# Kernel tuning notes

Hardware: AMD Instinct MI355X
Metric: run time of the kernel (lower is better)

Reference implementation:

```python
import jax, jax.numpy as jnp
import numpy as np

EPS = 1e-8


def householder_matrix(vs, dim):
    """Sequentially apply Householder reflections: Q <- (I - 2 v v^T / ||v||^2) Q."""
    def body(Q, v):
        coef = 2.0 / (jnp.sum(v * v) + EPS)
        Q = Q - coef * jnp.outer(v, v @ Q)
        return Q, None
    Q0 = jnp.eye(dim, dtype=vs.dtype)
    Q, _ = jax.lax.scan(body, Q0, vs)
    return Q


def _rotate_half(x):
    x1, x2 = jnp.split(x, 2, axis=-1)
    return jnp.concatenate((-x2, x1), axis=-1)


def setup_inputs() -> dict:
    key = jax.random.key(0)
    kq, kk, kc, ks, kv = jax.random.split(key, 5)
    B, H, S, D = 4, 16, 4096, 64
    q = jax.random.normal(kq, (B, H, S, D), dtype=jnp.float32)
    k = jax.random.normal(kk, (B, H, S, D), dtype=jnp.float32)
    cos = jax.random.uniform(kc, (B, S, D), dtype=jnp.float32)
    sin = jax.random.uniform(ks, (B, S, D), dtype=jnp.float32)
    vs = jax.random.normal(kv, (D // 2, D), dtype=jnp.float32) * 0.02
    return {"q": q, "k": k, "cos": cos, "sin": sin, "vs": vs}


def reference(q, k, cos, sin, vs):
    D = q.shape[-1]
    Q = householder_matrix(vs, D)            # [D, D], orthogonal
    # inverse rotation: x @ Q^T
    qi = q @ Q.T
    ki = k @ Q.T
    cos_b = cos[:, None, :, :]               # [B,1,S,D]
    sin_b = sin[:, None, :, :]
    q_rot = qi * cos_b + _rotate_half(qi) * sin_b
    k_rot = ki * cos_b + _rotate_half(ki) * sin_b
    # forward rotation: x @ Q
    return q_rot @ Q, k_rot @ Q
```

## Files before the change

### kernel.cpp

```cpp
#include <hip/hip_runtime.h>

typedef __attribute__((ext_vector_type(8))) short short8;
typedef __attribute__((ext_vector_type(4))) float floatx4;
typedef unsigned short u16;
typedef unsigned int   u32;

__device__ __forceinline__ u32 f2bf(float f) {
  u32 u = __float_as_uint(f);
  return (u + 0x7fffu + ((u >> 16) & 1u)) >> 16;
}

__device__ __forceinline__ short8 cvt8v(float4 a, float4 b) {
  short8 r;
  r[0] = (short)f2bf(a.x); r[1] = (short)f2bf(a.y); r[2] = (short)f2bf(a.z); r[3] = (short)f2bf(a.w);
  r[4] = (short)f2bf(b.x); r[5] = (short)f2bf(b.y); r[6] = (short)f2bf(b.z); r[7] = (short)f2bf(b.w);
  return r;
}

#define QB_OFF  0
#define QT_OFF  9216
#define COS_OFF 18432
#define SIN_OFF 22784
#define SH_OFF  27136
#define SV_OFF  18432

__global__ void __launch_bounds__(256, 4) rnrope_fused(
    const float* __restrict__ qp, const float* __restrict__ kp,
    const float* __restrict__ cosp, const float* __restrict__ sinp,
    const float* __restrict__ vsp, float* __restrict__ outp) {
  __shared__ __align__(16) char smem[36352];
  u16*   qb = (u16*)(smem + QB_OFF);
  u16*   qt = (u16*)(smem + QT_OFF);
  float* cs = (float*)(smem + COS_OFF);
  float* sn = (float*)(smem + SIN_OFF);
  float* sv = (float*)(smem + SV_OFF);

  const int tid  = threadIdx.x;
  const int lane = tid & 63;
  const int t    = lane & 15;
  const int quad = lane >> 4;
  const int wave = tid >> 6;
  u16* shw = (u16*)(smem + SH_OFF) + wave * 1152;

  const int b  = blockIdx.x >> 8;
  const int st = blockIdx.x & 255;
  const int s  = st << 4;

  *(float4*)(sv + tid * 8)     = *(const float4*)(vsp + tid * 8);
  *(float4*)(sv + tid * 8 + 4) = *(const float4*)(vsp + tid * 8 + 4);
  const int tk  = tid >> 4;
  const int off = (tid & 15) << 2;
  const float4 creg = *(const float4*)(cosp + (((b << 12) + s + tk) << 6) + off);
  const float4 sreg = *(const float4*)(sinp + (((b << 12) + s + tk) << 6) + off);
  __syncthreads();

  if (wave == 0) {
    const int j = lane;
    float col[64];
#pragma unroll
    for (int i = 0; i < 64; i++) col[i] = (i == j) ? 1.f : 0.f;
#pragma unroll 1
    for (int r = 0; r < 32; r++) {
      const float* vr = sv + r * 64;
      float vv0 = 0, vv1 = 0, vv2 = 0, vv3 = 0, w0 = 0, w1 = 0, w2 = 0, w3 = 0;
#pragma unroll
      for (int i = 0; i < 64; i += 4) {
        float4 v4 = *(const float4*)(vr + i);
        vv0 += v4.x * v4.x; vv1 += v4.y * v4.y; vv2 += v4.z * v4.z; vv3 += v4.w * v4.w;
        w0 += v4.x * col[i]; w1 += v4.y * col[i + 1]; w2 += v4.z * col[i + 2]; w3 += v4.w * col[i + 3];
      }
      float coef = 2.f / (((vv0 + vv1) + (vv2 + vv3)) + 1e-8f);
      float cw = coef * ((w0 + w1) + (w2 + w3));
#pragma unroll
      for (int i = 0; i < 64; i += 4) {
        float4 v4 = *(const float4*)(vr + i);
        col[i]     -= v4.x * cw;
        col[i + 1] -= v4.y * cw;
        col[i + 2] -= v4.z * cw;
        col[i + 3] -= v4.w * cw;
      }
    }
#pragma unroll
    for (int i = 0; i < 64; i += 2) {
      u16 v0 = (u16)f2bf(col[i]);
      u16 v1 = (u16)f2bf(col[i + 1]);
      qb[(i) * 72 + j]     = v0;
      qb[(i + 1) * 72 + j] = v1;
      *(u32*)&qt[j * 72 + i] = (u32)v0 | ((u32)v1 << 16);
    }
  }
  __syncthreads();
  *(float4*)(cs + tk * 68 + off) = creg;
  *(float4*)(sn + tk * 68 + off) = sreg;
  __syncthreads();

  const int hbase = b << 4;
  auto xptr = [&](int c) -> const float* {
    const float* base = (c < 16) ? qp : kp;
    return base + ((((hbase + (c & 15)) << 12) + s + t) << 6);
  };

  const int c0 = wave << 3;
  float4 n0, n1, n2, n3;
  {
    const float* p = xptr(c0);
    n0 = *(const float4*)(p + quad * 8);
    n1 = *(const float4*)(p + quad * 8 + 4);
    n2 = *(const float4*)(p + 32 + quad * 8);
    n3 = *(const float4*)(p + 32 + quad * 8 + 4);
  }

#pragma unroll 1
  for (int it = 0; it < 8; ++it) {
    const int c = c0 + it;
    float4 x0 = n0, x1 = n1, x2 = n2, x3 = n3;
    if (it < 7) {
      const float* p = xptr(c + 1);
      n0 = *(const float4*)(p + quad * 8);
      n1 = *(const float4*)(p + quad * 8 + 4);
      n2 = *(const float4*)(p + 32 + quad * 8);
      n3 = *(const float4*)(p + 32 + quad * 8 + 4);
    }
    short8 bq0 = cvt8v(x0, x1);
    short8 bq1 = cvt8v(x2, x3);

    int qoff = 0;
    asm volatile("" : "+v"(qoff));

    floatx4 acc[4];
#pragma unroll
    for (int i0 = 0; i0 < 4; i0++) {
      short8 a0 = *(const short8*)(qb + qoff + (i0 * 16 + t) * 72 + quad * 8);
      short8 a1 = *(const short8*)(qb + qoff + (i0 * 16 + t) * 72 + 32 + quad * 8);
      floatx4 z = {0.f, 0.f, 0.f, 0.f};
      z = __builtin_amdgcn_mfma_f32_16x16x32_bf16(a0, bq0, z, 0, 0, 0);
      z = __builtin_amdgcn_mfma_f32_16x16x32_bf16(a1, bq1, z, 0, 0, 0);
      acc[i0] = z;
    }

    float4 c4[4], s4[4];
#pragma unroll
    for (int i0 = 0; i0 < 4; i0++) {
      c4[i0] = *(const float4*)(cs + t * 68 + i0 * 16 + quad * 4);
      s4[i0] = *(const float4*)(sn + t * 68 + i0 * 16 + quad * 4);
    }
#pragma unroll
    for (int i0 = 0; i0 < 4; i0++) {
      const int p = i0 ^ 2;
      const float sg = (i0 < 2) ? -1.f : 1.f;
      float r0 = acc[i0][0] * c4[i0].x + sg * acc[p][0] * s4[i0].x;
      float r1 = acc[i0][1] * c4[i0].y + sg * acc[p][1] * s4[i0].y;
      float r2 = acc[i0][2] * c4[i0].z + sg * acc[p][2] * s4[i0].z;
      float r3 = acc[i0][3] * c4[i0].w + sg * acc[p][3] * s4[i0].w;
      u32 lo = f2bf(r0) | (f2bf(r1) << 16);
      u32 hi = f2bf(r2) | (f2bf(r3) << 16);
      *(uint2*)&shw[t * 72 + i0 * 16 + quad * 4] = make_uint2(lo, hi);
    }

    __builtin_amdgcn_wave_barrier();
    short8 br0 = *(const short8*)&shw[t * 72 + quad * 8];
    short8 br1 = *(const short8*)&shw[t * 72 + 32 + quad * 8];

    float* op = outp + ((c < 16) ? 0 : 16777216) + ((((hbase + (c & 15)) << 12) + s + t) << 6);
#pragma unroll
    for (int o0 = 0; o0 < 4; o0++) {
      short8 a0 = *(const short8*)(qt + qoff + (o0 * 16 + t) * 72 + quad * 8);
      short8 a1 = *(const short8*)(qt + qoff + (o0 * 16 + t) * 72 + 32 + quad * 8);
      floatx4 z = {0.f, 0.f, 0.f, 0.f};
      z = __builtin_amdgcn_mfma_f32_16x16x32_bf16(a0, br0, z, 0, 0, 0);
      z = __builtin_amdgcn_mfma_f32_16x16x32_bf16(a1, br1, z, 0, 0, 0);
      *(float4*)(op + o0 * 16 + quad * 4) = make_float4(z[0], z[1], z[2], z[3]);
    }
    __builtin_amdgcn_wave_barrier();
  }
}

extern "C" void kernel_launch(void* const* d_in, const int* in_sizes, int n_in,
                              void* d_out, int out_size, void* d_ws, size_t ws_size,
                              hipStream_t stream) {
  const float* q    = (const float*)d_in[0];
  const float* k    = (const float*)d_in[1];
  const float* cosp = (const float*)d_in[2];
  const float* sinp = (const float*)d_in[3];
  const float* vs   = (const float*)d_in[4];
  float* out = (float*)d_out;
  hipLaunchKernelGGL(rnrope_fused, dim3(1024), dim3(256), 0, stream,
                     q, k, cosp, sinp, vs, out);
}
```

Measured before the change: 304.9 us.

## Split Householder build across four waves and keep cos/sin in registers

The per-block Householder matrix construction was done by one wave with 64-element columns while the other three waves idled. It is now split across all four waves, each holding a 16-row segment, with partial dot products reduced through double-buffered shared memory and a block barrier per reflection. Cos/sin are loaded directly into registers once instead of being staged in LDS and reloaded each iteration. This shrinks LDS and allows occupancy 5. The cost is 32 extra __syncthreads and more live registers for cos/sin.

```diff
diff --git a/kernel.cpp b/kernel.cpp
--- a/kernel.cpp
+++ b/kernel.cpp
@@ -19,21 +19,21 @@
 
 #define QB_OFF  0
 #define QT_OFF  9216
-#define COS_OFF 18432
-#define SIN_OFF 22784
-#define SH_OFF  27136
+#define SH_OFF  18432
 #define SV_OFF  18432
+#define PW_OFF  27648
+#define PV_OFF  29696
 
-__global__ void __launch_bounds__(256, 4) rnrope_fused(
+__global__ void __launch_bounds__(256, 5) rnrope_fused(
     const float* __restrict__ qp, const float* __restrict__ kp,
     const float* __restrict__ cosp, const float* __restrict__ sinp,
     const float* __restrict__ vsp, float* __restrict__ outp) {
-  __shared__ __align__(16) char smem[36352];
+  __shared__ __align__(16) char smem[29728];
   u16*   qb = (u16*)(smem + QB_OFF);
   u16*   qt = (u16*)(smem + QT_OFF);
-  float* cs = (float*)(smem + COS_OFF);
-  float* sn = (float*)(smem + SIN_OFF);
   float* sv = (float*)(smem + SV_OFF);
+  float* pw = (float*)(smem + PW_OFF);
+  float* pv = (float*)(smem + PV_OFF);
 
   const int tid  = threadIdx.x;
   const int lane = tid & 63;
@@ -42,57 +42,71 @@
   const int wave = tid >> 6;
   u16* shw = (u16*)(smem + SH_OFF) + wave * 1152;
 
-  const int b  = blockIdx.x >> 8;
-  const int st = blockIdx.x & 255;
-  const int s  = st << 4;
+  const int b = blockIdx.x >> 8;
+  const int s = (blockIdx.x & 255) << 4;
 
   *(float4*)(sv + tid * 8)     = *(const float4*)(vsp + tid * 8);
   *(float4*)(sv + tid * 8 + 4) = *(const float4*)(vsp + tid * 8 + 4);
-  const int tk  = tid >> 4;
-  const int off = (tid & 15) << 2;
-  const float4 creg = *(const float4*)(cosp + (((b << 12) + s + tk) << 6) + off);
-  const float4 sreg = *(const float4*)(sinp + (((b << 12) + s + tk) << 6) + off);
   __syncthreads();
 
-  if (wave == 0) {
-    const int j = lane;
-    float col[64];
+  const int j   = lane;
+  const int seg = wave;
+  float col16[16];
 #pragma unroll
-    for (int i = 0; i < 64; i++) col[i] = (i == j) ? 1.f : 0.f;
+  for (int i = 0; i < 16; i++) col16[i] = (seg * 16 + i == j) ? 1.f : 0.f;
+
 #pragma unroll 1
-    for (int r = 0; r < 32; r++) {
-      const float* vr = sv + r * 64;
-      float vv0 = 0, vv1 = 0, vv2 = 0, vv3 = 0, w0 = 0, w1 = 0, w2 = 0, w3 = 0;
+  for (int r = 0; r < 32; r++) {
+    const float* vr = sv + r * 64 + seg * 16;
+    float4 va = *(const float4*)(vr);
+    float4 vb = *(const float4*)(vr + 4);
+    float4 vc = *(const float4*)(vr + 8);
+    float4 vd = *(const float4*)(vr + 12);
+    float w = va.x * col16[0]  + va.y * col16[1]  + va.z * col16[2]  + va.w * col16[3]
+            + vb.x * col16[4]  + vb.y * col16[5]  + vb.z * col16[6]  + vb.w * col16[7]
+            + vc.x * col16[8]  + vc.y * col16[9]  + vc.z * col16[10] + vc.w * col16[11]
+            + vd.x * col16[12] + vd.y * col16[13] + vd.z * col16[14] + vd.w * col16[15];
+    float vvp = va.x * va.x + va.y * va.y + va.z * va.z + va.w * va.w
+              + vb.x * vb.x + vb.y * vb.y + vb.z * vb.z + vb.w * vb.w
+              + vc.x * vc.x + vc.y * vc.y + vc.z * vc.z + vc.w * vc.w
+              + vd.x * vd.x + vd.y * vd.y + vd.z * vd.z + vd.w * vd.w;
+    const int par = (r & 1);
+    pw[par * 256 + seg * 64 + j] = w;
+    if (j == 0) pv[par * 4 + seg] = vvp;
+    __syncthreads();
+    const float* pwr = pw + par * 256;
+    const float* pvr = pv + par * 4;
+    float wsum = (pwr[j] + pwr[64 + j]) + (pwr[128 + j] + pwr[192 + j]);
+    float vv   = (pvr[0] + pvr[1]) + (pvr[2] + pvr[3]);
+    float cw = (2.f / (vv + 1e-8f)) * wsum;
+    col16[0]  -= va.x * cw; col16[1]  -= va.y * cw; col16[2]  -= va.z * cw; col16[3]  -= va.w * cw;
+    col16[4]  -= vb.x * cw; col16[5]  -= vb.y * cw; col16[6]  -= vb.z * cw; col16[7]  -= vb.w * cw;
+    col16[8]  -= vc.x * cw; col16[9]  -= vc.y * cw; col16[10] -= vc.z * cw; col16[11] -= vc.w * cw;
+    col16[12] -= vd.x * cw; col16[13] -= vd.y * cw; col16[14] -= vd.z * cw; col16[15] -= vd.w * cw;
+  }
+
 #pragma unroll
-      for (int i = 0; i < 64; i += 4) {
-        float4 v4 = *(const float4*)(vr + i);
-        vv0 += v4.x * v4.x; vv1 += v4.y * v4.y; vv2 += v4.z * v4.z; vv3 += v4.w * v4.w;
-        w0 += v4.x * col[i]; w1 += v4.y * col[i + 1]; w2 += v4.z * col[i + 2]; w3 += v4.w * col[i + 3];
-      }
-      float coef = 2.f / (((vv0 + vv1) + (vv2 + vv3)) + 1e-8f);
-      float cw = coef * ((w0 + w1) + (w2 + w3));
+  for (int i = 0; i < 16; i++) qb[(seg * 16 + i) * 72 + j] = (u16)f2bf(col16[i]);
+  {
+    u32 pk[8];
 #pragma unroll
-      for (int i = 0; i < 64; i += 4) {
-        float4 v4 = *(const float4*)(vr + i);
-        col[i]     -= v4.x * cw;
-        col[i + 1] -= v4.y * cw;
-        col[i + 2] -= v4.z * cw;
-        col[i + 3] -= v4.w * cw;
-      }
-    }
-#pragma unroll
-    for (int i = 0; i < 64; i += 2) {
-      u16 v0 = (u16)f2bf(col[i]);
-      u16 v1 = (u16)f2bf(col[i + 1]);
-      qb[(i) * 72 + j]     = v0;
-      qb[(i + 1) * 72 + j] = v1;
-      *(u32*)&qt[j * 72 + i] = (u32)v0 | ((u32)v1 << 16);
-    }
+    for (int i = 0; i < 8; i++) pk[i] = f2bf(col16[2 * i]) | (f2bf(col16[2 * i + 1]) << 16);
+    u16* qtr = qt + j * 72 + seg * 16;
+    *(uint2*)(qtr)      = make_uint2(pk[0], pk[1]);
+    *(uint2*)(qtr + 4)  = make_uint2(pk[2], pk[3]);
+    *(uint2*)(qtr + 8)  = make_uint2(pk[4], pk[5]);
+    *(uint2*)(qtr + 12) = make_uint2(pk[6], pk[7]);
   }
   __syncthreads();
-  *(float4*)(cs + tk * 68 + off) = creg;
-  *(float4*)(sn + tk * 68 + off) = sreg;
-  __syncthreads();
+
+  const float* crow = cosp + (((b << 12) + s + t) << 6);
+  const float* srow = sinp + (((b << 12) + s + t) << 6);
+  float4 c4[4], s4[4];
+#pragma unroll
+  for (int i0 = 0; i0 < 4; i0++) {
+    c4[i0] = *(const float4*)(crow + i0 * 16 + quad * 4);
+    s4[i0] = *(const float4*)(srow + i0 * 16 + quad * 4);
+  }
 
   const int hbase = b << 4;
   auto xptr = [&](int c) -> const float* {
@@ -138,12 +152,6 @@
       acc[i0] = z;
     }
 
-    float4 c4[4], s4[4];
-#pragma unroll
-    for (int i0 = 0; i0 < 4; i0++) {
-      c4[i0] = *(const float4*)(cs + t * 68 + i0 * 16 + quad * 4);
-      s4[i0] = *(const float4*)(sn + t * 68 + i0 * 16 + quad * 4);
-    }
 #pragma unroll
     for (int i0 = 0; i0 < 4; i0++) {
       const int p = i0 ^ 2;
```

New measurement: 262.4 us. 13.9% less time.
